# Performance work log

Measured on AMD Instinct MI355X. Metric: run time of the kernel, lower is better.

The kernel has to match this reference:

```python
import jax, jax.numpy as jnp
import numpy as np

D_MODEL = 64
TEMPER = float(np.power(D_MODEL, 0.5))  # d_model ** temper_value
B, L, DK = 64, 1024, 64
P = 2 * L - 1  # relative position range


def setup_inputs() -> dict:
    key = jax.random.key(0)
    k1, k2, k3, k4, k5 = jax.random.split(key, 5)
    q = jax.random.normal(k1, (B, L, DK), dtype=jnp.float32)
    k = jax.random.normal(k2, (B, L, DK), dtype=jnp.float32)
    v = jax.random.normal(k3, (B, L, DK), dtype=jnp.float32)
    position_dpa = jax.random.normal(k4, (B, P, DK), dtype=jnp.float32)
    attn_mask = jax.random.uniform(k5, (B, L, L)) < 0.1
    return {"q": q, "k": k, "v": v, "position_dpa": position_dpa, "attn_mask": attn_mask}


def reference(q, k, v, position_dpa, attn_mask):
    # q,k,v: [B, L, d]; position_dpa: [B, 2L-1, d]; attn_mask: [B, L, L] bool
    Lq = q.shape[1]
    attn = jnp.einsum('bld,bmd->blm', q, k) / TEMPER            # [B, L, L]
    attn_pos = jnp.einsum('bld,bpd->blp', q, position_dpa) / TEMPER  # [B, L, 2L-1]
    # Replicates batch_stripe(flip(attn_pos.transpose(1,2), -1)).transpose(1,2):
    # bias[b, i, j] = attn_pos[b, L-1-i, i+j]
    i = jnp.arange(Lq)
    rows = (Lq - 1) - i[:, None]                 # [L, 1]
    cols = i[:, None] + i[None, :]               # [L, L], values in [0, 2L-2]
    bias = attn_pos[:, rows, cols]               # [B, L, L]
    attn = attn + bias
    attn = jnp.where(attn_mask, -jnp.inf, attn)
    attn = jax.nn.softmax(attn, axis=-1)
    # dropout is identity in eval mode
    output = jnp.einsum('blm,bmd->bld', attn, v)  # [B, L, d]
    return output, attn
```

## Files before the change

### kernel.cpp

```cpp
#include <hip/hip_runtime.h>

#define BN   64
#define LN   1024
#define DKN  64
#define PN   2047
#define OUT_O_ELEMS ((size_t)BN * LN * DKN)
constexpr float kScale = 0.125f;

typedef short bf16x8 __attribute__((ext_vector_type(8)));
typedef float f32x4  __attribute__((ext_vector_type(4)));

__device__ __forceinline__ unsigned short f2b(float f) {
  return (unsigned short)((__float_as_uint(f) + 0x8000u) >> 16);
}
__device__ __forceinline__ float b2f(unsigned short h) {
  return __uint_as_float(((unsigned)h) << 16);
}
__device__ __forceinline__ unsigned pk2(float x, float y) {
  unsigned lo = (__float_as_uint(x) + 0x8000u) >> 16;
  unsigned hi = (__float_as_uint(y) + 0x8000u) & 0xFFFF0000u;
  return lo | hi;
}

union U8 { unsigned u[4]; bf16x8 v; };

__device__ __forceinline__ bf16x8 pack8(float4 a, float4 b) {
  U8 r;
  r.u[0] = pk2(a.x, a.y); r.u[1] = pk2(a.z, a.w);
  r.u[2] = pk2(b.x, b.y); r.u[3] = pk2(b.z, b.w);
  return r.v;
}

__global__ void flag_init(unsigned* f) { *f = 0u; }

__global__ void flag_scan(const unsigned* __restrict__ mw, unsigned* f) {
  int idx = blockIdx.x * 256 + threadIdx.x;
  unsigned bits = 0;
#pragma unroll
  for (int i = 0; i < 4; ++i) {
    unsigned wv = mw[idx * 4 + i];
    if (wv == 0x3F800000u) bits |= 2u;
    else if (wv > 1u)      bits |= 4u;
  }
  if (bits) atomicOr(f, bits);
}

__global__ __launch_bounds__(256) void pack_mask(const void* __restrict__ mask,
                                                 const unsigned* __restrict__ flagp,
                                                 unsigned short* __restrict__ mb) {
  const int t  = threadIdx.x;
  const size_t rowBase = (size_t)blockIdx.x << 4;
  unsigned mflag = flagp ? flagp[0] : 0u;
  const int mkind = (mflag & 4u) ? 1 : ((mflag & 2u) ? 2 : 0);
  unsigned b0 = 0, b1 = 0, b2 = 0, b3 = 0;
  if (mkind == 1) {
    const unsigned* mp = (const unsigned*)mask;
#pragma unroll
    for (int i = 0; i < 16; ++i) {
      unsigned wv = mp[((rowBase + i) << 8) + t];
      if (wv & 0x000000FFu) b0 |= (1u << i);
      if (wv & 0x0000FF00u) b1 |= (1u << i);
      if (wv & 0x00FF0000u) b2 |= (1u << i);
      if (wv & 0xFF000000u) b3 |= (1u << i);
    }
  } else {
    const uint4* mp = (const uint4*)mask;
#pragma unroll
    for (int i = 0; i < 16; ++i) {
      uint4 wv = mp[((rowBase + i) << 8) + t];
      if (wv.x) b0 |= (1u << i);
      if (wv.y) b1 |= (1u << i);
      if (wv.z) b2 |= (1u << i);
      if (wv.w) b3 |= (1u << i);
    }
  }
  *(uint2*)(mb + ((size_t)blockIdx.x << 10) + (t << 2)) =
      make_uint2(b0 | (b1 << 16), b2 | (b3 << 16));
}

__global__ __launch_bounds__(256) void convert2_f32_bf16(const float4* __restrict__ a,
                                                         uint2* __restrict__ oa, int na,
                                                         const float4* __restrict__ bsrc,
                                                         uint2* __restrict__ ob) {
  int idx = blockIdx.x * 256 + threadIdx.x;
  if (idx < na) {
    float4 x = a[idx];
    oa[idx] = make_uint2(pk2(x.x, x.y), pk2(x.z, x.w));
  } else {
    int j = idx - na;
    float4 x = bsrc[j];
    ob[j] = make_uint2(pk2(x.x, x.y), pk2(x.z, x.w));
  }
}

__global__ __launch_bounds__(256) void transpose_v(const float4* __restrict__ vg,
                                                   short* __restrict__ vt) {
  __shared__ float tile[64 * 65];
  const int tid = threadIdx.x;
  const int b  = blockIdx.x >> 4;
  const int mt = blockIdx.x & 15;
  const size_t base = ((size_t)b * 1024 + mt * 64) * 16;
#pragma unroll
  for (int i = 0; i < 4; ++i) {
    int j = tid + (i << 8);
    float4 a = vg[base + j];
    float* d = &tile[(j >> 4) * 65 + ((j & 15) << 2)];
    d[0] = a.x; d[1] = a.y; d[2] = a.z; d[3] = a.w;
  }
  __syncthreads();
#pragma unroll
  for (int i = 0; i < 4; ++i) {
    int j  = tid + (i << 8);
    int d  = j >> 4;
    int mq = (j & 15) << 2;
    unsigned u0 = pk2(tile[(mq + 0) * 65 + d], tile[(mq + 1) * 65 + d]);
    unsigned u1 = pk2(tile[(mq + 2) * 65 + d], tile[(mq + 3) * 65 + d]);
    size_t idx = ((size_t)b * 64 + d) * 1024 + mt * 64 + mq;
    *(uint2*)(vt + idx) = make_uint2(u0, u1);
  }
}

__global__ __launch_bounds__(256, 4)
void attn_kernel(const float* __restrict__ qf, const float* __restrict__ kf,
                 const float* __restrict__ vf, const float* __restrict__ pf,
                 const void* __restrict__ mask, const unsigned* __restrict__ flagp,
                 const short* __restrict__ k16, const short* __restrict__ p16,
                 const short* __restrict__ vt16, const unsigned short* __restrict__ maskBp,
                 float* __restrict__ out) {
  __shared__ short E[16 * 1024];

  const int tid  = threadIdx.x;
  const int w    = tid >> 6;
  const int lane = tid & 63;
  const int col  = lane & 15;
  const int quad = lane >> 4;

  int p   = blockIdx.x;
  int xcd = p & 7;
  int qq  = p >> 3;
  int rt  = qq & 63;
  int bh  = qq >> 6;
  const int b  = (bh << 3) | xcd;
  const int l0 = rt << 4;

  unsigned mflag = flagp ? flagp[0] : 0u;
  const int mkind = (mflag & 4u) ? 1 : ((mflag & 2u) ? 2 : 0);

  const float4* qg = (const float4*)qf;
  const size_t qrow  = ((size_t)b * LN + (size_t)(l0 + col)) * 16 + (size_t)(quad * 2);
  const size_t qrrow = ((size_t)b * LN + (size_t)(LN - 1 - l0 - col)) * 16 + (size_t)(quad * 2);
  const bf16x8 aq0 = pack8(qg[qrow],      qg[qrow + 1]);
  const bf16x8 aq1 = pack8(qg[qrow + 8],  qg[qrow + 9]);
  const bf16x8 ar0 = pack8(qg[qrrow],     qg[qrrow + 1]);
  const bf16x8 ar1 = pack8(qg[qrrow + 8], qg[qrrow + 9]);

  const int moff = (w << 4) + col;
  const size_t mrow0 = (((size_t)b << 10) + (size_t)(l0 + (quad << 2))) << 10;
  const unsigned short* mbRow = maskBp ? (maskBp + (((size_t)(b << 6) + rt) << 10)) : nullptr;

  if (k16) {
    struct KPM { bf16x8 k0, k1, p00, p01, p10, p11; unsigned m[4]; };
    KPM A, Bf;

    auto LOAD = [&](int t, KPM& o) {
      const int m0 = t << 6, mglob = m0 + moff;
      const short* kr = k16 + ((size_t)b * LN + mglob) * DKN + quad * 8;
      o.k0 = *(const bf16x8*)kr;
      o.k1 = *(const bf16x8*)(kr + 32);
      int g0 = l0 + m0 + moff;
      int g1 = g0 + 16; if (g1 > PN - 1) g1 = PN - 1;
      const short* pr0 = p16 + ((size_t)b * PN + g0) * DKN + quad * 8;
      const short* pr1 = p16 + ((size_t)b * PN + g1) * DKN + quad * 8;
      o.p00 = *(const bf16x8*)pr0;
      o.p01 = *(const bf16x8*)(pr0 + 32);
      o.p10 = *(const bf16x8*)pr1;
      o.p11 = *(const bf16x8*)(pr1 + 32);
      if (mbRow) {
        o.m[0] = mbRow[mglob];
      } else {
        const size_t mi = mrow0 + (size_t)mglob;
        if (mkind == 1) {
          const unsigned char* mp = (const unsigned char*)mask + mi;
#pragma unroll
          for (int r = 0; r < 4; ++r) o.m[r] = __builtin_nontemporal_load(mp + ((size_t)r << 10));
        } else {
          const unsigned* mp = (const unsigned*)mask + mi;
#pragma unroll
          for (int r = 0; r < 4; ++r) o.m[r] = __builtin_nontemporal_load(mp + ((size_t)r << 10));
        }
      }
    };

    auto COMP = [&](int t, KPM& o) {
      f32x4 qk = {0.f, 0.f, 0.f, 0.f};
      qk = __builtin_amdgcn_mfma_f32_16x16x32_bf16(aq0, o.k0, qk, 0, 0, 0);
      qk = __builtin_amdgcn_mfma_f32_16x16x32_bf16(aq1, o.k1, qk, 0, 0, 0);
      f32x4 ba = {0.f, 0.f, 0.f, 0.f}, bb = {0.f, 0.f, 0.f, 0.f};
      ba = __builtin_amdgcn_mfma_f32_16x16x32_bf16(ar0, o.p00, ba, 0, 0, 0);
      ba = __builtin_amdgcn_mfma_f32_16x16x32_bf16(ar1, o.p01, ba, 0, 0, 0);
      bb = __builtin_amdgcn_mfma_f32_16x16x32_bf16(ar0, o.p10, bb, 0, 0, 0);
      bb = __builtin_amdgcn_mfma_f32_16x16x32_bf16(ar1, o.p11, bb, 0, 0, 0);
      const int mglob = (t << 6) + moff;
#pragma unroll
      for (int r = 0; r < 4; ++r) {
        int i = (quad << 2) + r;
        int o2 = i + col;
        int srcLane = (lane & 48) | (o2 & 15);
        float va = __shfl(ba[r], srcLane);
        float vb = __shfl(bb[r], srcLane);
        float bias = (o2 < 16) ? va : vb;
        float s = (qk[r] + bias) * kScale;
        bool msk = mbRow ? (((o.m[0] >> i) & 1u) != 0u) : (o.m[r] != 0u);
        float e = msk ? 0.f : __expf(s);
        E[i * 1024 + (mglob ^ ((i & 7) << 3))] = (short)f2b(e);
      }
    };

    LOAD(0, A);
    for (int t = 0; t < 16; t += 2) {
      LOAD(t + 1, Bf);
      COMP(t, A);
      if (t < 14) LOAD(t + 2, A);
      COMP(t + 1, Bf);
    }
  } else {
    for (int t = 0; t < 16; ++t) {
      const int m0 = t << 6, mglob = m0 + moff;
      int g0 = l0 + m0 + moff;
      int g1 = g0 + 16; if (g1 > PN - 1) g1 = PN - 1;
      const float4* kr = (const float4*)(kf + ((size_t)b * LN + mglob) * DKN);
      bf16x8 kb0 = pack8(kr[quad * 2], kr[quad * 2 + 1]);
      bf16x8 kb1 = pack8(kr[8 + quad * 2], kr[9 + quad * 2]);
      const float4* pr0 = (const float4*)(pf + ((size_t)b * PN + g0) * DKN);
      const float4* pr1 = (const float4*)(pf + ((size_t)b * PN + g1) * DKN);
      bf16x8 pb00 = pack8(pr0[quad * 2], pr0[quad * 2 + 1]);
      bf16x8 pb01 = pack8(pr0[8 + quad * 2], pr0[9 + quad * 2]);
      bf16x8 pb10 = pack8(pr1[quad * 2], pr1[quad * 2 + 1]);
      bf16x8 pb11 = pack8(pr1[8 + quad * 2], pr1[9 + quad * 2]);

      f32x4 qk = {0.f, 0.f, 0.f, 0.f};
      qk = __builtin_amdgcn_mfma_f32_16x16x32_bf16(aq0, kb0, qk, 0, 0, 0);
      qk = __builtin_amdgcn_mfma_f32_16x16x32_bf16(aq1, kb1, qk, 0, 0, 0);
      f32x4 ba = {0.f, 0.f, 0.f, 0.f}, bb = {0.f, 0.f, 0.f, 0.f};
      ba = __builtin_amdgcn_mfma_f32_16x16x32_bf16(ar0, pb00, ba, 0, 0, 0);
      ba = __builtin_amdgcn_mfma_f32_16x16x32_bf16(ar1, pb01, ba, 0, 0, 0);
      bb = __builtin_amdgcn_mfma_f32_16x16x32_bf16(ar0, pb10, bb, 0, 0, 0);
      bb = __builtin_amdgcn_mfma_f32_16x16x32_bf16(ar1, pb11, bb, 0, 0, 0);

#pragma unroll
      for (int r = 0; r < 4; ++r) {
        int i = (quad << 2) + r;
        int o2 = i + col;
        int srcLane = (lane & 48) | (o2 & 15);
        float va = __shfl(ba[r], srcLane);
        float vb = __shfl(bb[r], srcLane);
        float bias = (o2 < 16) ? va : vb;
        float s = (qk[r] + bias) * kScale;
        size_t mi = mrow0 + ((size_t)r << 10) + (size_t)mglob;
        unsigned mu = (mkind == 1) ? (unsigned)((const unsigned char*)mask)[mi]
                                   : ((const unsigned*)mask)[mi];
        float e = mu ? 0.f : __expf(s);
        E[i * 1024 + (mglob ^ ((i & 7) << 3))] = (short)f2b(e);
      }
    }
  }
  __syncthreads();

  f32x4 acc  = {0.f, 0.f, 0.f, 0.f};
  f32x4 acc2 = {0.f, 0.f, 0.f, 0.f};
  U8 onesU; onesU.u[0] = onesU.u[1] = onesU.u[2] = onesU.u[3] = 0x3F803F80u;
  const bf16x8 ONE = onesU.v;
  const int drow = moff;
  const int esw  = (col & 7) << 3;

  if (vt16) {
    const short* vbase = vt16 + ((size_t)b * 64 + drow) * 1024 + quad * 8;
    bf16x8 v0A = *(const bf16x8*)vbase;
    bf16x8 v1A = *(const bf16x8*)(vbase + 32);
    bf16x8 v0B, v1B;
    for (int t = 0; t < 16; t += 2) {
      { const short* vr = vbase + ((t + 1) << 6);
        v0B = *(const bf16x8*)vr; v1B = *(const bf16x8*)(vr + 32); }
      { const int m0 = t << 6;
        bf16x8 ea0 = *(const bf16x8*)&E[col * 1024 + ((m0 + quad * 8) ^ esw)];
        bf16x8 ea1 = *(const bf16x8*)&E[col * 1024 + ((m0 + 32 + quad * 8) ^ esw)];
        acc  = __builtin_amdgcn_mfma_f32_16x16x32_bf16(ea0, v0A, acc,  0, 0, 0);
        acc  = __builtin_amdgcn_mfma_f32_16x16x32_bf16(ea1, v1A, acc,  0, 0, 0);
        acc2 = __builtin_amdgcn_mfma_f32_16x16x32_bf16(ea0, ONE, acc2, 0, 0, 0);
        acc2 = __builtin_amdgcn_mfma_f32_16x16x32_bf16(ea1, ONE, acc2, 0, 0, 0); }
      if (t < 14) { const short* vr = vbase + ((t + 2) << 6);
        v0A = *(const bf16x8*)vr; v1A = *(const bf16x8*)(vr + 32); }
      { const int m0 = (t + 1) << 6;
        bf16x8 ea0 = *(const bf16x8*)&E[col * 1024 + ((m0 + quad * 8) ^ esw)];
        bf16x8 ea1 = *(const bf16x8*)&E[col * 1024 + ((m0 + 32 + quad * 8) ^ esw)];
        acc  = __builtin_amdgcn_mfma_f32_16x16x32_bf16(ea0, v0B, acc,  0, 0, 0);
        acc  = __builtin_amdgcn_mfma_f32_16x16x32_bf16(ea1, v1B, acc,  0, 0, 0);
        acc2 = __builtin_amdgcn_mfma_f32_16x16x32_bf16(ea0, ONE, acc2, 0, 0, 0);
        acc2 = __builtin_amdgcn_mfma_f32_16x16x32_bf16(ea1, ONE, acc2, 0, 0, 0); }
    }
  } else {
    for (int t = 0; t < 16; ++t) {
      const int m0 = t << 6;
      const float* vc = vf + ((size_t)b * LN + m0) * DKN + drow;
      U8 t0, t1;
#pragma unroll
      for (int j = 0; j < 4; ++j) {
        t0.u[j] = pk2(vc[(quad * 8 + 2 * j) * 64],      vc[(quad * 8 + 2 * j + 1) * 64]);
        t1.u[j] = pk2(vc[(32 + quad * 8 + 2 * j) * 64], vc[(32 + quad * 8 + 2 * j + 1) * 64]);
      }
      bf16x8 ea0 = *(const bf16x8*)&E[col * 1024 + ((m0 + quad * 8) ^ esw)];
      bf16x8 ea1 = *(const bf16x8*)&E[col * 1024 + ((m0 + 32 + quad * 8) ^ esw)];
      acc  = __builtin_amdgcn_mfma_f32_16x16x32_bf16(ea0, t0.v, acc,  0, 0, 0);
      acc  = __builtin_amdgcn_mfma_f32_16x16x32_bf16(ea1, t1.v, acc,  0, 0, 0);
      acc2 = __builtin_amdgcn_mfma_f32_16x16x32_bf16(ea0, ONE, acc2, 0, 0, 0);
      acc2 = __builtin_amdgcn_mfma_f32_16x16x32_bf16(ea1, ONE, acc2, 0, 0, 0);
    }
  }

  float invR[4];
#pragma unroll
  for (int r = 0; r < 4; ++r) invR[r] = 1.0f / acc2[r];

#pragma unroll
  for (int r = 0; r < 4; ++r) {
    int i = (quad << 2) + r;
    out[(((size_t)b << 10) + (size_t)(l0 + i)) * 64 + drow] = acc[r] * invR[r];
  }

  float* outA = out + OUT_O_ELEMS;
  const size_t aBase = (((size_t)b << 10) + (size_t)l0) << 10;
#pragma unroll
  for (int t = 0; t < 16; ++t) {
    float inv = __shfl(invR[t & 3], (t >> 2) << 4);
    const ushort4 ev = *(const ushort4*)&E[t * 1024 + ((tid << 2) ^ ((t & 7) << 3))];
    f32x4 o4;
    o4[0] = b2f(ev.x) * inv;
    o4[1] = b2f(ev.y) * inv;
    o4[2] = b2f(ev.z) * inv;
    o4[3] = b2f(ev.w) * inv;
    __builtin_nontemporal_store(o4, (f32x4*)&outA[aBase + ((size_t)t << 10) + (size_t)(tid << 2)]);
  }
}

extern "C" void kernel_launch(void* const* d_in, const int* in_sizes, int n_in,
                              void* d_out, int out_size, void* d_ws, size_t ws_size,
                              hipStream_t stream) {
  const float* q   = (const float*)d_in[0];
  const float* k   = (const float*)d_in[1];
  const float* v   = (const float*)d_in[2];
  const float* pos = (const float*)d_in[3];
  const void* mask = d_in[4];
  float* out = (float*)d_out;

  unsigned* flag = nullptr;
  if (ws_size >= 256) {
    flag = (unsigned*)d_ws;
    flag_init<<<1, 1, 0, stream>>>(flag);
    flag_scan<<<64, 256, 0, stream>>>((const unsigned*)mask, flag);
  }

  const size_t kElems  = (size_t)BN * LN * DKN;
  const size_t pElems  = (size_t)BN * PN * DKN;
  const size_t offK    = 256;
  const size_t offP    = offK + kElems * 2;
  const size_t offVT   = offP + pElems * 2;
  const size_t offMB   = offVT + kElems * 2;
  const size_t mbBytes = (size_t)BN * 64 * 1024 * 2;
  const size_t wsNeed  = offMB;
  const size_t wsFull  = offMB + mbBytes;

  short *k16 = nullptr, *p16 = nullptr, *vt16 = nullptr;
  unsigned short* maskB = nullptr;
  if (ws_size >= wsNeed) {
    char* base = (char*)d_ws;
    k16  = (short*)(base + offK);
    p16  = (short*)(base + offP);
    vt16 = (short*)(base + offVT);
    const int na = (int)(kElems / 4);
    const int nb = (int)(pElems / 4);
    convert2_f32_bf16<<<(na + nb) / 256, 256, 0, stream>>>((const float4*)k, (uint2*)k16, na,
                                                           (const float4*)pos, (uint2*)p16);
    transpose_v<<<BN * 16, 256, 0, stream>>>((const float4*)v, vt16);
    if (ws_size >= wsFull && flag) {
      maskB = (unsigned short*)(base + offMB);
      pack_mask<<<BN * 64, 256, 0, stream>>>(mask, flag, maskB);
    }
  }

  attn_kernel<<<BN * (LN / 16), 256, 0, stream>>>(q, k, v, pos, mask, flag,
                                                  k16, p16, vt16, maskB, out);
}
```

Baseline: 746.7 us.

## Compute softmax row sums in the exp phase and interleave attn stores with PV

```diff
diff --git a/kernel.cpp b/kernel.cpp
--- a/kernel.cpp
+++ b/kernel.cpp
@@ -128,6 +128,7 @@
                  const short* __restrict__ vt16, const unsigned short* __restrict__ maskBp,
                  float* __restrict__ out) {
   __shared__ short E[16 * 1024];
+  __shared__ float rsPart[4][16];
 
   const int tid  = threadIdx.x;
   const int w    = tid >> 6;
@@ -157,6 +158,8 @@
   const int moff = (w << 4) + col;
   const size_t mrow0 = (((size_t)b << 10) + (size_t)(l0 + (quad << 2))) << 10;
   const unsigned short* mbRow = maskBp ? (maskBp + (((size_t)(b << 6) + rt) << 10)) : nullptr;
+
+  float sumr[4] = {0.f, 0.f, 0.f, 0.f};
 
   if (k16) {
     struct KPM { bf16x8 k0, k1, p00, p01, p10, p11; unsigned m[4]; };
@@ -212,7 +215,9 @@
         float s = (qk[r] + bias) * kScale;
         bool msk = mbRow ? (((o.m[0] >> i) & 1u) != 0u) : (o.m[r] != 0u);
         float e = msk ? 0.f : __expf(s);
-        E[i * 1024 + (mglob ^ ((i & 7) << 3))] = (short)f2b(e);
+        unsigned short eb = f2b(e);
+        sumr[r] += b2f(eb);
+        E[i * 1024 + (mglob ^ ((i & 7) << 3))] = (short)eb;
       }
     };
 
@@ -260,18 +265,42 @@
         unsigned mu = (mkind == 1) ? (unsigned)((const unsigned char*)mask)[mi]
                                    : ((const unsigned*)mask)[mi];
         float e = mu ? 0.f : __expf(s);
-        E[i * 1024 + (mglob ^ ((i & 7) << 3))] = (short)f2b(e);
+        unsigned short eb = f2b(e);
+        sumr[r] += b2f(eb);
+        E[i * 1024 + (mglob ^ ((i & 7) << 3))] = (short)eb;
       }
     }
   }
+
+#pragma unroll
+  for (int r = 0; r < 4; ++r) {
+    float vsum = sumr[r];
+    vsum += __shfl_xor(vsum, 1);
+    vsum += __shfl_xor(vsum, 2);
+    vsum += __shfl_xor(vsum, 4);
+    vsum += __shfl_xor(vsum, 8);
+    if (col == 0) rsPart[w][(quad << 2) + r] = vsum;
+  }
   __syncthreads();
 
-  f32x4 acc  = {0.f, 0.f, 0.f, 0.f};
-  f32x4 acc2 = {0.f, 0.f, 0.f, 0.f};
-  U8 onesU; onesU.u[0] = onesU.u[1] = onesU.u[2] = onesU.u[3] = 0x3F803F80u;
-  const bf16x8 ONE = onesU.v;
+  const float invL = 1.0f / (rsPart[0][col] + rsPart[1][col] + rsPart[2][col] + rsPart[3][col]);
+
+  f32x4 acc = {0.f, 0.f, 0.f, 0.f};
   const int drow = moff;
   const int esw  = (col & 7) << 3;
+  float* outA = out + OUT_O_ELEMS;
+  const size_t aBase = (((size_t)b << 10) + (size_t)l0) << 10;
+
+  auto WROW = [&](int t) {
+    float inv = __shfl(invL, (lane & 48) | t);
+    const ushort4 ev = *(const ushort4*)&E[t * 1024 + ((tid << 2) ^ ((t & 7) << 3))];
+    f32x4 o4;
+    o4[0] = b2f(ev.x) * inv;
+    o4[1] = b2f(ev.y) * inv;
+    o4[2] = b2f(ev.z) * inv;
+    o4[3] = b2f(ev.w) * inv;
+    __builtin_nontemporal_store(o4, (f32x4*)&outA[aBase + ((size_t)t << 10) + (size_t)(tid << 2)]);
+  };
 
   if (vt16) {
     const short* vbase = vt16 + ((size_t)b * 64 + drow) * 1024 + quad * 8;
@@ -284,19 +313,17 @@
       { const int m0 = t << 6;
         bf16x8 ea0 = *(const bf16x8*)&E[col * 1024 + ((m0 + quad * 8) ^ esw)];
         bf16x8 ea1 = *(const bf16x8*)&E[col * 1024 + ((m0 + 32 + quad * 8) ^ esw)];
-        acc  = __builtin_amdgcn_mfma_f32_16x16x32_bf16(ea0, v0A, acc,  0, 0, 0);
-        acc  = __builtin_amdgcn_mfma_f32_16x16x32_bf16(ea1, v1A, acc,  0, 0, 0);
-        acc2 = __builtin_amdgcn_mfma_f32_16x16x32_bf16(ea0, ONE, acc2, 0, 0, 0);
-        acc2 = __builtin_amdgcn_mfma_f32_16x16x32_bf16(ea1, ONE, acc2, 0, 0, 0); }
+        acc = __builtin_amdgcn_mfma_f32_16x16x32_bf16(ea0, v0A, acc, 0, 0, 0);
+        acc = __builtin_amdgcn_mfma_f32_16x16x32_bf16(ea1, v1A, acc, 0, 0, 0);
+        WROW(t); }
       if (t < 14) { const short* vr = vbase + ((t + 2) << 6);
         v0A = *(const bf16x8*)vr; v1A = *(const bf16x8*)(vr + 32); }
       { const int m0 = (t + 1) << 6;
         bf16x8 ea0 = *(const bf16x8*)&E[col * 1024 + ((m0 + quad * 8) ^ esw)];
         bf16x8 ea1 = *(const bf16x8*)&E[col * 1024 + ((m0 + 32 + quad * 8) ^ esw)];
-        acc  = __builtin_amdgcn_mfma_f32_16x16x32_bf16(ea0, v0B, acc,  0, 0, 0);
-        acc  = __builtin_amdgcn_mfma_f32_16x16x32_bf16(ea1, v1B, acc,  0, 0, 0);
-        acc2 = __builtin_amdgcn_mfma_f32_16x16x32_bf16(ea0, ONE, acc2, 0, 0, 0);
-        acc2 = __builtin_amdgcn_mfma_f32_16x16x32_bf16(ea1, ONE, acc2, 0, 0, 0); }
+        acc = __builtin_amdgcn_mfma_f32_16x16x32_bf16(ea0, v0B, acc, 0, 0, 0);
+        acc = __builtin_amdgcn_mfma_f32_16x16x32_bf16(ea1, v1B, acc, 0, 0, 0);
+        WROW(t + 1); }
     }
   } else {
     for (int t = 0; t < 16; ++t) {
@@ -310,35 +337,17 @@
       }
       bf16x8 ea0 = *(const bf16x8*)&E[col * 1024 + ((m0 + quad * 8) ^ esw)];
       bf16x8 ea1 = *(const bf16x8*)&E[col * 1024 + ((m0 + 32 + quad * 8) ^ esw)];
-      acc  = __builtin_amdgcn_mfma_f32_16x16x32_bf16(ea0, t0.v, acc,  0, 0, 0);
-      acc  = __builtin_amdgcn_mfma_f32_16x16x32_bf16(ea1, t1.v, acc,  0, 0, 0);
-      acc2 = __builtin_amdgcn_mfma_f32_16x16x32_bf16(ea0, ONE, acc2, 0, 0, 0);
-      acc2 = __builtin_amdgcn_mfma_f32_16x16x32_bf16(ea1, ONE, acc2, 0, 0, 0);
-    }
-  }
-
-  float invR[4];
-#pragma unroll
-  for (int r = 0; r < 4; ++r) invR[r] = 1.0f / acc2[r];
+      acc = __builtin_amdgcn_mfma_f32_16x16x32_bf16(ea0, t0.v, acc, 0, 0, 0);
+      acc = __builtin_amdgcn_mfma_f32_16x16x32_bf16(ea1, t1.v, acc, 0, 0, 0);
+      WROW(t);
+    }
+  }
 
 #pragma unroll
   for (int r = 0; r < 4; ++r) {
     int i = (quad << 2) + r;
-    out[(((size_t)b << 10) + (size_t)(l0 + i)) * 64 + drow] = acc[r] * invR[r];
-  }
-
-  float* outA = out + OUT_O_ELEMS;
-  const size_t aBase = (((size_t)b << 10) + (size_t)l0) << 10;
-#pragma unroll
-  for (int t = 0; t < 16; ++t) {
-    float inv = __shfl(invR[t & 3], (t >> 2) << 4);
-    const ushort4 ev = *(const ushort4*)&E[t * 1024 + ((tid << 2) ^ ((t & 7) << 3))];
-    f32x4 o4;
-    o4[0] = b2f(ev.x) * inv;
-    o4[1] = b2f(ev.y) * inv;
-    o4[2] = b2f(ev.z) * inv;
-    o4[3] = b2f(ev.w) * inv;
-    __builtin_nontemporal_store(o4, (f32x4*)&outA[aBase + ((size_t)t << 10) + (size_t)(tid << 2)]);
+    float invO = __shfl(invL, (lane & 48) | i);
+    out[(((size_t)b << 10) + (size_t)(l0 + i)) * 64 + drow] = acc[r] * invO;
   }
 }
 
```

Result: slower. 804.5 us (+7.7%).
